# Kernel tuning notes

Measured on AMD Instinct MI355X. Metric: run time of the kernel, lower is better.

The kernel has to match this reference:

```python
import jax, jax.numpy as jnp
import numpy as np

B, S, H = 2, 2048, 1024
NH, HD = 16, 64  # num heads, head dim
EPS = 1e-12


def setup_inputs() -> dict:
    key = jax.random.key(0)
    ks = jax.random.split(key, 10)
    scale = 0.02
    return {
        "hidden_states": jax.random.normal(ks[0], (B, S, H), jnp.float32),
        "attention_mask": jnp.zeros((B, 1, 1, S), jnp.float32),
        "Wq": jax.random.normal(ks[1], (H, H), jnp.float32) * scale,
        "bq": jnp.zeros((H,), jnp.float32),
        "Wk": jax.random.normal(ks[2], (H, H), jnp.float32) * scale,
        "bk": jnp.zeros((H,), jnp.float32),
        "Wv": jax.random.normal(ks[3], (H, H), jnp.float32) * scale,
        "bv": jnp.zeros((H,), jnp.float32),
        "Wo": jax.random.normal(ks[4], (H, H), jnp.float32) * scale,
        "bo": jnp.zeros((H,), jnp.float32),
        "ln_gamma": jnp.ones((H,), jnp.float32),
        "ln_beta": jnp.zeros((H,), jnp.float32),
    }


def _split_heads(x):
    # [B,S,H] -> [B,NH,S,HD]
    b, s, _ = x.shape
    return x.reshape(b, s, NH, HD).transpose(0, 2, 1, 3)


def reference(hidden_states, attention_mask, Wq, bq, Wk, bk, Wv, bv, Wo, bo, ln_gamma, ln_beta):
    q = _split_heads(hidden_states @ Wq + bq)
    k = _split_heads(hidden_states @ Wk + bk)
    v = _split_heads(hidden_states @ Wv + bv)

    # unfused SDPA, as in source: matmul -> scale -> mask -> softmax -> matmul
    scores = jnp.einsum('bhqd,bhkd->bhqk', q, k) / jnp.sqrt(jnp.float32(HD))
    scores = scores + attention_mask
    probs = jax.nn.softmax(scores, axis=-1)  # dropout p=0 (eval)
    ctx = jnp.einsum('bhqk,bhkd->bhqd', probs, v)
    ctx = ctx.transpose(0, 2, 1, 3).reshape(hidden_states.shape)  # [B,S,H]

    # BaseBertSelfOutput: dense -> (dropout p=0) -> LayerNorm(residual)
    out = ctx @ Wo + bo
    res = out + hidden_states
    mu = jnp.mean(res, axis=-1, keepdims=True)
    var = jnp.mean(jnp.square(res - mu), axis=-1, keepdims=True)
    normed = (res - mu) * jax.lax.rsqrt(var + EPS)
    return normed * ln_gamma + ln_beta
```

## Files before the change

kernel.cpp:

```cpp
#include <hip/hip_runtime.h>
#include <hip/hip_bf16.h>

#define B_  2
#define S_  2048
#define H_  1024
#define NH_ 16
#define HD_ 64
#define EPSLN 1e-12f
#define LOG2E 1.4426950408889634f

typedef short bf16x8 __attribute__((ext_vector_type(8)));
typedef float f32x4  __attribute__((ext_vector_type(4)));

__device__ __forceinline__ float bf2f(ushort u) {
    union { unsigned int i; float f; } v; v.i = ((unsigned int)u) << 16; return v.f;
}
__device__ __forceinline__ ushort f2bf(float f) {
    union { float f; unsigned int i; } v; v.f = f;
    unsigned int r = v.i + 0x7FFFu + ((v.i >> 16) & 1u);
    return (ushort)(r >> 16);
}
__device__ __forceinline__ ushort f2bf_hw(float f) {
    __hip_bfloat16 h = __float2bfloat16(f);
    return *reinterpret_cast<ushort*>(&h);
}
__device__ __forceinline__ unsigned int pack_bf2(float a, float b) {
    return ((unsigned int)f2bf_hw(b) << 16) | (unsigned int)f2bf_hw(a);
}

__global__ __launch_bounds__(256) void cvt_f32_bf16(const float* __restrict__ in,
                                                    ushort* __restrict__ out, int n) {
    int i = (blockIdx.x * 256 + threadIdx.x) * 4;
    float4 v = *(const float4*)&in[i];
    ushort4 o = make_ushort4(f2bf(v.x), f2bf(v.y), f2bf(v.z), f2bf(v.w));
    *(ushort4*)&out[i] = o;
}

__global__ __launch_bounds__(256) void scale_mask(const float* __restrict__ in,
                                                  float* __restrict__ out) {
    int i = blockIdx.x * 256 + threadIdx.x;
    out[i] = in[i] * LOG2E;
}

__global__ __launch_bounds__(256) void transpose_cvt(
        const float* __restrict__ W0, const float* __restrict__ W1,
        const float* __restrict__ W2, const float* __restrict__ W3,
        ushort* __restrict__ T0, ushort* __restrict__ T1,
        ushort* __restrict__ T2, ushort* __restrict__ T3) {
    const int z = blockIdx.z;
    const float* in = (z == 0) ? W0 : (z == 1) ? W1 : (z == 2) ? W2 : W3;
    ushort* out     = (z == 0) ? T0 : (z == 1) ? T1 : (z == 2) ? T2 : T3;

    __shared__ float tile[64][65];
    const int bx = blockIdx.x * 64, by = blockIdx.y * 64;
    const int t = threadIdx.x;
    #pragma unroll
    for (int i = 0; i < 16; i++) {
        int idx = t + i * 256;
        int r = idx >> 6, c = idx & 63;
        tile[r][c] = in[(by + r) * 1024 + bx + c];
    }
    __syncthreads();
    #pragma unroll
    for (int i = 0; i < 16; i++) {
        int idx = t + i * 256;
        int r = idx >> 6, c = idx & 63;
        out[(bx + r) * 1024 + by + c] = f2bf(tile[c][r]);
    }
}

__global__ __launch_bounds__(256) void v_transpose(const ushort* __restrict__ Vb,
                                                   ushort* __restrict__ VtG) {
    __shared__ ushort tile[64][72];
    const int s0 = blockIdx.x * 64;
    const int head = blockIdx.y;
    const ushort* src = Vb + (size_t)head * S_ * HD_;
    ushort* dst       = VtG + (size_t)head * S_ * HD_;
    const int t = threadIdx.x, lane = t & 63, w = t >> 6;

    uint4 a = *(const uint4*)&src[(s0 + lane) * HD_ + w * 16];
    uint4 b = *(const uint4*)&src[(s0 + lane) * HD_ + w * 16 + 8];
    const ushort* pa = (const ushort*)&a;
    #pragma unroll
    for (int i = 0; i < 8; i++) tile[w * 16 + i][lane] = pa[i];
    const ushort* pb = (const ushort*)&b;
    #pragma unroll
    for (int i = 0; i < 8; i++) tile[w * 16 + 8 + i][lane] = pb[i];
    __syncthreads();

    const int d = t >> 2, sc = (t & 3) * 16;
    uint4 o1 = *(const uint4*)&tile[d][sc];
    uint4 o2 = *(const uint4*)&tile[d][sc + 8];
    *(uint4*)&dst[d * S_ + s0 + sc]     = o1;
    *(uint4*)&dst[d * S_ + s0 + sc + 8] = o2;
}

__global__ __launch_bounds__(256) void qkv_gemm(
        const ushort* __restrict__ X,
        const ushort* __restrict__ Wqt, const ushort* __restrict__ Wkt, const ushort* __restrict__ Wvt,
        const float* __restrict__ bq,  const float* __restrict__ bk,  const float* __restrict__ bv,
        ushort* __restrict__ Qo, ushort* __restrict__ Ko, ushort* __restrict__ Vo) {
    const int which = blockIdx.z;
    const ushort* Wt  = (which == 0) ? Wqt : (which == 1) ? Wkt : Wvt;
    const float* bias = (which == 0) ? bq  : (which == 1) ? bk  : bv;
    ushort* Out       = (which == 0) ? Qo  : (which == 1) ? Ko  : Vo;

    __shared__ ushort As[128][72];
    __shared__ ushort Bs[128][72];
    const int m0 = blockIdx.x * 128, n0 = blockIdx.y * 128;
    const int t = threadIdx.x;
    const int lane = t & 63, w = t >> 6;
    const int wr = (w >> 1) * 64, wc = (w & 1) * 64;
    const int l15 = lane & 15, l4 = lane >> 4;

    f32x4 acc[4][4] = {};
    const int sr = t >> 3, sc = (t & 7) * 8;

    for (int k0 = 0; k0 < H_; k0 += 64) {
        __syncthreads();
        #pragma unroll
        for (int p = 0; p < 4; p++) {
            uint4 av  = *(const uint4*)&X [(m0 + p * 32 + sr) * H_ + k0 + sc];
            uint4 bv2 = *(const uint4*)&Wt[(n0 + p * 32 + sr) * H_ + k0 + sc];
            *(uint4*)&As[p * 32 + sr][sc] = av;
            *(uint4*)&Bs[p * 32 + sr][sc] = bv2;
        }
        __syncthreads();
        #pragma unroll
        for (int ks = 0; ks < 2; ks++) {
            bf16x8 af[4], bfr[4];
            #pragma unroll
            for (int i = 0; i < 4; i++) af[i]  = *(const bf16x8*)&As[wr + i * 16 + l15][ks * 32 + l4 * 8];
            #pragma unroll
            for (int i = 0; i < 4; i++) bfr[i] = *(const bf16x8*)&Bs[wc + i * 16 + l15][ks * 32 + l4 * 8];
            #pragma unroll
            for (int mi = 0; mi < 4; mi++)
                #pragma unroll
                for (int ni = 0; ni < 4; ni++)
                    acc[mi][ni] = __builtin_amdgcn_mfma_f32_16x16x32_bf16(af[mi], bfr[ni], acc[mi][ni], 0, 0, 0);
        }
    }

    #pragma unroll
    for (int ni = 0; ni < 4; ni++) {
        int n = n0 + wc + ni * 16 + l15;
        float bvf = bias[n];
        int h = n >> 6, d = n & 63;
        #pragma unroll
        for (int mi = 0; mi < 4; mi++) {
            int mrow = m0 + wr + mi * 16 + l4 * 4;
            #pragma unroll
            for (int j = 0; j < 4; j++) {
                int m = mrow + j;
                int b = m >> 11, s = m & 2047;
                Out[((b * NH_ + h) * S_ + s) * HD_ + d] = f2bf(acc[mi][ni][j] + bvf);
            }
        }
    }
}

__global__ __launch_bounds__(256) void flash_attn(
        const ushort* __restrict__ Q, const ushort* __restrict__ K, const ushort* __restrict__ VtG,
        const float* __restrict__ maskL2, ushort* __restrict__ ctx) {
    __shared__ __align__(16) ushort Ks[64][72];
    __shared__ __align__(16) ushort Vt[64][72];
    __shared__ __align__(16) ushort Ps[4][16][72];

    const int wgid = blockIdx.x;
    const int vid  = (wgid & 7) * 128 + (wgid >> 3);
    const int qt   = vid & 31;
    const int hb   = vid >> 5;
    const int h    = hb & (NH_ - 1), b = hb >> 4;

    const int t = threadIdx.x, lane = t & 63, w = t >> 6;
    const int l15 = lane & 15, l4 = lane >> 4;
    const size_t head_off = (size_t)hb * S_ * HD_;
    const ushort* Qh = Q + head_off;
    const ushort* Kh = K + head_off;
    const ushort* Vh = VtG + head_off;

    const int qrow = qt * 64 + w * 16 + l15;
    bf16x8 qf[2];
    qf[0] = *(const bf16x8*)&Qh[qrow * 64 + 0  + l4 * 8];
    qf[1] = *(const bf16x8*)&Qh[qrow * 64 + 32 + l4 * 8];

    f32x4 ctx_acc[4] = {};
    float mrun = -1e30f, lrun = 0.f;

    const int sr  = t >> 2, sc0 = (t & 3) * 8;
    const int vsc = (t & 3) * 16;

    uint4 kr0 = *(const uint4*)&Kh[sr * 64 + sc0];
    uint4 kr1 = *(const uint4*)&Kh[sr * 64 + sc0 + 32];
    uint4 vr0 = *(const uint4*)&Vh[sr * S_ + vsc];
    uint4 vr1 = *(const uint4*)&Vh[sr * S_ + vsc + 8];

    const float ksc = 0.125f * LOG2E;

    for (int kv0 = 0; kv0 < S_; kv0 += 64) {
        __syncthreads();
        *(uint4*)&Ks[sr][sc0]      = kr0;
        *(uint4*)&Ks[sr][sc0 + 32] = kr1;
        *(uint4*)&Vt[sr][vsc]      = vr0;
        *(uint4*)&Vt[sr][vsc + 8]  = vr1;
        if (kv0 + 64 < S_) {
            kr0 = *(const uint4*)&Kh[(kv0 + 64 + sr) * 64 + sc0];
            kr1 = *(const uint4*)&Kh[(kv0 + 64 + sr) * 64 + sc0 + 32];
            vr0 = *(const uint4*)&Vh[sr * S_ + kv0 + 64 + vsc];
            vr1 = *(const uint4*)&Vh[sr * S_ + kv0 + 64 + vsc + 8];
        }
        __syncthreads();

        f32x4 sacc[4] = {};
        #pragma unroll
        for (int ks = 0; ks < 2; ks++) {
            bf16x8 kf[4];
            #pragma unroll
            for (int n = 0; n < 4; n++) kf[n] = *(const bf16x8*)&Ks[n * 16 + l15][ks * 32 + l4 * 8];
            #pragma unroll
            for (int n = 0; n < 4; n++)
                sacc[n] = __builtin_amdgcn_mfma_f32_16x16x32_bf16(kf[n], qf[ks], sacc[n], 0, 0, 0);
        }

        float tmax = -1e30f;
        #pragma unroll
        for (int n = 0; n < 4; n++) {
            float4 mk4 = *(const float4*)&maskL2[b * S_ + kv0 + n * 16 + l4 * 4];
            sacc[n][0] = fmaf(sacc[n][0], ksc, mk4.x);
            sacc[n][1] = fmaf(sacc[n][1], ksc, mk4.y);
            sacc[n][2] = fmaf(sacc[n][2], ksc, mk4.z);
            sacc[n][3] = fmaf(sacc[n][3], ksc, mk4.w);
            tmax = fmaxf(tmax, fmaxf(fmaxf(sacc[n][0], sacc[n][1]), fmaxf(sacc[n][2], sacc[n][3])));
        }
        tmax = fmaxf(tmax, __shfl_xor(tmax, 16, 64));
        tmax = fmaxf(tmax, __shfl_xor(tmax, 32, 64));

        float mnew  = fmaxf(mrun, tmax);
        float scale = exp2f(mrun - mnew);
        mrun = mnew;

        float tsum = 0.f;
        #pragma unroll
        for (int n = 0; n < 4; n++) {
            float p0 = exp2f(sacc[n][0] - mnew);
            float p1 = exp2f(sacc[n][1] - mnew);
            float p2 = exp2f(sacc[n][2] - mnew);
            float p3 = exp2f(sacc[n][3] - mnew);
            tsum += (p0 + p1) + (p2 + p3);
            uint2 pw = make_uint2(pack_bf2(p0, p1), pack_bf2(p2, p3));
            *(uint2*)&Ps[w][l15][n * 16 + l4 * 4] = pw;
        }
        tsum += __shfl_xor(tsum, 16, 64);
        tsum += __shfl_xor(tsum, 32, 64);
        lrun = lrun * scale + tsum;

        float sj[4];
        #pragma unroll
        for (int j = 0; j < 4; j++) sj[j] = __shfl(scale, l4 * 4 + j, 64);
        #pragma unroll
        for (int df = 0; df < 4; df++)
            #pragma unroll
            for (int j = 0; j < 4; j++) ctx_acc[df][j] *= sj[j];

        #pragma unroll
        for (int ks = 0; ks < 2; ks++) {
            bf16x8 pf = *(const bf16x8*)&Ps[w][l15][ks * 32 + l4 * 8];
            #pragma unroll
            for (int df = 0; df < 4; df++) {
                bf16x8 vf = *(const bf16x8*)&Vt[df * 16 + l15][ks * 32 + l4 * 8];
                ctx_acc[df] = __builtin_amdgcn_mfma_f32_16x16x32_bf16(pf, vf, ctx_acc[df], 0, 0, 0);
            }
        }
    }

    float lr[4];
    #pragma unroll
    for (int j = 0; j < 4; j++) lr[j] = 1.0f / __shfl(lrun, l4 * 4 + j, 64);
    #pragma unroll
    for (int df = 0; df < 4; df++) {
        int col = h * HD_ + df * 16 + l15;
        #pragma unroll
        for (int j = 0; j < 4; j++) {
            int s = qt * 64 + w * 16 + l4 * 4 + j;
            ctx[((size_t)b * S_ + s) * H_ + col] = f2bf(ctx_acc[df][j] * lr[j]);
        }
    }
}

__global__ __launch_bounds__(256) void out_proj(
        const ushort* __restrict__ Ctx, const ushort* __restrict__ Wot,
        const float* __restrict__ bo,  const float* __restrict__ Hs,
        float* __restrict__ Tmp) {
    __shared__ ushort As[128][72];
    __shared__ ushort Bs[128][72];
    const int m0 = blockIdx.x * 128, n0 = blockIdx.y * 128;
    const int t = threadIdx.x;
    const int lane = t & 63, w = t >> 6;
    const int wr = (w >> 1) * 64, wc = (w & 1) * 64;
    const int l15 = lane & 15, l4 = lane >> 4;

    f32x4 acc[4][4] = {};
    const int sr = t >> 3, sc = (t & 7) * 8;

    for (int k0 = 0; k0 < H_; k0 += 64) {
        __syncthreads();
        #pragma unroll
        for (int p = 0; p < 4; p++) {
            uint4 av  = *(const uint4*)&Ctx[(m0 + p * 32 + sr) * H_ + k0 + sc];
            uint4 bv2 = *(const uint4*)&Wot[(n0 + p * 32 + sr) * H_ + k0 + sc];
            *(uint4*)&As[p * 32 + sr][sc] = av;
            *(uint4*)&Bs[p * 32 + sr][sc] = bv2;
        }
        __syncthreads();
        #pragma unroll
        for (int ks = 0; ks < 2; ks++) {
            bf16x8 af[4], bfr[4];
            #pragma unroll
            for (int i = 0; i < 4; i++) af[i]  = *(const bf16x8*)&As[wr + i * 16 + l15][ks * 32 + l4 * 8];
            #pragma unroll
            for (int i = 0; i < 4; i++) bfr[i] = *(const bf16x8*)&Bs[wc + i * 16 + l15][ks * 32 + l4 * 8];
            #pragma unroll
            for (int mi = 0; mi < 4; mi++)
                #pragma unroll
                for (int ni = 0; ni < 4; ni++)
                    acc[mi][ni] = __builtin_amdgcn_mfma_f32_16x16x32_bf16(af[mi], bfr[ni], acc[mi][ni], 0, 0, 0);
        }
    }

    #pragma unroll
    for (int ni = 0; ni < 4; ni++) {
        int n = n0 + wc + ni * 16 + l15;
        float bvf = bo[n];
        #pragma unroll
        for (int mi = 0; mi < 4; mi++) {
            int mrow = m0 + wr + mi * 16 + l4 * 4;
            #pragma unroll
            for (int j = 0; j < 4; j++) {
                int m = mrow + j;
                Tmp[(size_t)m * H_ + n] = acc[mi][ni][j] + bvf + Hs[(size_t)m * H_ + n];
            }
        }
    }
}

__global__ __launch_bounds__(256) void ln_kernel(
        const float* __restrict__ Tmp, const float* __restrict__ gamma,
        const float* __restrict__ beta, float* __restrict__ Out) {
    const int row = blockIdx.x;
    const float* x = Tmp + (size_t)row * H_;
    const int t = threadIdx.x, w = t >> 6, lane = t & 63;

    float4 v = *(const float4*)&x[t * 4];
    float s = v.x + v.y + v.z + v.w;
    #pragma unroll
    for (int m = 1; m < 64; m <<= 1) s += __shfl_xor(s, m, 64);
    __shared__ float red[4], red2[4];
    if (lane == 0) red[w] = s;
    __syncthreads();
    float mu = (red[0] + red[1] + red[2] + red[3]) * (1.0f / H_);

    float d0 = v.x - mu, d1 = v.y - mu, d2 = v.z - mu, d3 = v.w - mu;
    float sq = d0 * d0 + d1 * d1 + d2 * d2 + d3 * d3;
    #pragma unroll
    for (int m = 1; m < 64; m <<= 1) sq += __shfl_xor(sq, m, 64);
    if (lane == 0) red2[w] = sq;
    __syncthreads();
    float var = (red2[0] + red2[1] + red2[2] + red2[3]) * (1.0f / H_);
    float rstd = rsqrtf(var + EPSLN);

    float dd[4] = {d0, d1, d2, d3};
    float4 o;
    o.x = dd[0] * rstd * gamma[t * 4 + 0] + beta[t * 4 + 0];
    o.y = dd[1] * rstd * gamma[t * 4 + 1] + beta[t * 4 + 1];
    o.z = dd[2] * rstd * gamma[t * 4 + 2] + beta[t * 4 + 2];
    o.w = dd[3] * rstd * gamma[t * 4 + 3] + beta[t * 4 + 3];
    *(float4*)&Out[(size_t)row * H_ + t * 4] = o;
}

extern "C" void kernel_launch(void* const* d_in, const int* in_sizes, int n_in,
                              void* d_out, int out_size, void* d_ws, size_t ws_size,
                              hipStream_t stream) {
    const float* hs    = (const float*)d_in[0];
    const float* mask  = (const float*)d_in[1];
    const float* Wq    = (const float*)d_in[2];
    const float* bq    = (const float*)d_in[3];
    const float* Wk    = (const float*)d_in[4];
    const float* bk    = (const float*)d_in[5];
    const float* Wv    = (const float*)d_in[6];
    const float* bv    = (const float*)d_in[7];
    const float* Wo    = (const float*)d_in[8];
    const float* bo    = (const float*)d_in[9];
    const float* gamma = (const float*)d_in[10];
    const float* beta  = (const float*)d_in[11];

    char* ws = (char*)d_ws;
    const size_t WSZ = (size_t)H_ * H_;
    const size_t TSZ = (size_t)B_ * S_ * H_;
    ushort* Wqt = (ushort*)ws;
    ushort* Wkt = Wqt + WSZ;
    ushort* Wvt = Wkt + WSZ;
    ushort* Wot = Wvt + WSZ;
    ushort* Xb  = Wot + WSZ;
    ushort* Qb  = Xb + TSZ;
    ushort* Kb  = Qb + TSZ;
    ushort* Vb  = Kb + TSZ;
    ushort* Ctx = Vb + TSZ;
    float*  Tmp = (float*)(Ctx + TSZ);
    ushort* VtG = (ushort*)Tmp;
    float* MaskL2 = (float*)Xb;

    cvt_f32_bf16<<<TSZ / (256 * 4), 256, 0, stream>>>(hs, Xb, (int)TSZ);
    transpose_cvt<<<dim3(16, 16, 4), 256, 0, stream>>>(Wq, Wk, Wv, Wo, Wqt, Wkt, Wvt, Wot);

    qkv_gemm<<<dim3(32, 8, 3), 256, 0, stream>>>(Xb, Wqt, Wkt, Wvt, bq, bk, bv, Qb, Kb, Vb);
    scale_mask<<<(B_ * S_) / 256, 256, 0, stream>>>(mask, MaskL2);
    v_transpose<<<dim3(S_ / 64, B_ * NH_), 256, 0, stream>>>(Vb, VtG);
    flash_attn<<<dim3(1024), 256, 0, stream>>>(Qb, Kb, VtG, MaskL2, Ctx);
    out_proj<<<dim3(32, 8), 256, 0, stream>>>(Ctx, Wot, bo, hs, Tmp);
    ln_kernel<<<B_ * S_, 256, 0, stream>>>(Tmp, gamma, beta, (float*)d_out);
}
```

Before: 176.0 us.

## Rewrite flash attention with 32x32 MFMA, register-resident P, and lazy rescaling

Flash attention now uses 32x32x16 MFMA tiles with 2 waves of 32 query rows each (128 threads) instead of 4 waves using 16x16 tiles. The probability tile is passed from the QK^T accumulator to the PV MFMA operand through cross-lane shuffles rather than a round trip through shared memory. The running max is only rescaled when a tile's max exceeds it by more than 8 (log2 units), which skips most accumulator rescales. The intent is to cut LDS traffic, shuffles and VALU work per KV tile. In exchange there is more register pressure, half as many threads per block, and larger unnormalised exponentials (bounded by 2^8).

After: 287.3 us. +63.2%, slower.

```diff
diff --git a/kernel.cpp b/kernel.cpp
--- a/kernel.cpp
+++ b/kernel.cpp
@@ -11,6 +11,8 @@
 
 typedef short bf16x8 __attribute__((ext_vector_type(8)));
 typedef float f32x4  __attribute__((ext_vector_type(4)));
+typedef float f32x16 __attribute__((ext_vector_type(16)));
+typedef unsigned int u32x4 __attribute__((ext_vector_type(4)));
 
 __device__ __forceinline__ float bf2f(ushort u) {
     union { unsigned int i; float f; } v; v.i = ((unsigned int)u) << 16; return v.f;
@@ -159,12 +161,11 @@
     }
 }
 
-__global__ __launch_bounds__(256) void flash_attn(
+__global__ __launch_bounds__(128) void flash_attn(
         const ushort* __restrict__ Q, const ushort* __restrict__ K, const ushort* __restrict__ VtG,
         const float* __restrict__ maskL2, ushort* __restrict__ ctx) {
     __shared__ __align__(16) ushort Ks[64][72];
     __shared__ __align__(16) ushort Vt[64][72];
-    __shared__ __align__(16) ushort Ps[4][16][72];
 
     const int wgid = blockIdx.x;
     const int vid  = (wgid & 7) * 128 + (wgid >> 3);
@@ -173,117 +174,138 @@
     const int h    = hb & (NH_ - 1), b = hb >> 4;
 
     const int t = threadIdx.x, lane = t & 63, w = t >> 6;
-    const int l15 = lane & 15, l4 = lane >> 4;
+    const int l31 = lane & 31, hi = lane >> 5;
     const size_t head_off = (size_t)hb * S_ * HD_;
     const ushort* Qh = Q + head_off;
     const ushort* Kh = K + head_off;
     const ushort* Vh = VtG + head_off;
 
-    const int qrow = qt * 64 + w * 16 + l15;
-    bf16x8 qf[2];
-    qf[0] = *(const bf16x8*)&Qh[qrow * 64 + 0  + l4 * 8];
-    qf[1] = *(const bf16x8*)&Qh[qrow * 64 + 32 + l4 * 8];
-
-    f32x4 ctx_acc[4] = {};
+    const int q0w  = qt * 64 + w * 32;
+    const int qrow = q0w + l31;
+    bf16x8 qf[4];
+    #pragma unroll
+    for (int kc = 0; kc < 4; kc++)
+        qf[kc] = *(const bf16x8*)&Qh[qrow * 64 + kc * 16 + hi * 8];
+
+    f32x16 acc0 = {}, acc1 = {};
     float mrun = -1e30f, lrun = 0.f;
 
-    const int sr  = t >> 2, sc0 = (t & 3) * 8;
-    const int vsc = (t & 3) * 16;
-
-    uint4 kr0 = *(const uint4*)&Kh[sr * 64 + sc0];
-    uint4 kr1 = *(const uint4*)&Kh[sr * 64 + sc0 + 32];
-    uint4 vr0 = *(const uint4*)&Vh[sr * S_ + vsc];
-    uint4 vr1 = *(const uint4*)&Vh[sr * S_ + vsc + 8];
+    uint4 kpre[4], vpre[4];
+    #pragma unroll
+    for (int it = 0; it < 4; it++) {
+        int ci = it * 128 + t;
+        int row = ci >> 3, ce = (ci & 7) * 8;
+        kpre[it] = *(const uint4*)&Kh[row * 64 + ce];
+        vpre[it] = *(const uint4*)&Vh[row * S_ + ce];
+    }
 
     const float ksc = 0.125f * LOG2E;
 
     for (int kv0 = 0; kv0 < S_; kv0 += 64) {
         __syncthreads();
-        *(uint4*)&Ks[sr][sc0]      = kr0;
-        *(uint4*)&Ks[sr][sc0 + 32] = kr1;
-        *(uint4*)&Vt[sr][vsc]      = vr0;
-        *(uint4*)&Vt[sr][vsc + 8]  = vr1;
+        #pragma unroll
+        for (int it = 0; it < 4; it++) {
+            int ci = it * 128 + t;
+            int row = ci >> 3, ce = (ci & 7) * 8;
+            *(uint4*)&Ks[row][ce] = kpre[it];
+            *(uint4*)&Vt[row][ce] = vpre[it];
+        }
         if (kv0 + 64 < S_) {
-            kr0 = *(const uint4*)&Kh[(kv0 + 64 + sr) * 64 + sc0];
-            kr1 = *(const uint4*)&Kh[(kv0 + 64 + sr) * 64 + sc0 + 32];
-            vr0 = *(const uint4*)&Vh[sr * S_ + kv0 + 64 + vsc];
-            vr1 = *(const uint4*)&Vh[sr * S_ + kv0 + 64 + vsc + 8];
-        }
-        __syncthreads();
-
-        f32x4 sacc[4] = {};
-        #pragma unroll
-        for (int ks = 0; ks < 2; ks++) {
-            bf16x8 kf[4];
-            #pragma unroll
-            for (int n = 0; n < 4; n++) kf[n] = *(const bf16x8*)&Ks[n * 16 + l15][ks * 32 + l4 * 8];
-            #pragma unroll
-            for (int n = 0; n < 4; n++)
-                sacc[n] = __builtin_amdgcn_mfma_f32_16x16x32_bf16(kf[n], qf[ks], sacc[n], 0, 0, 0);
+            #pragma unroll
+            for (int it = 0; it < 4; it++) {
+                int ci = it * 128 + t;
+                int row = ci >> 3, ce = (ci & 7) * 8;
+                kpre[it] = *(const uint4*)&Kh[(kv0 + 64 + row) * 64 + ce];
+                vpre[it] = *(const uint4*)&Vh[row * S_ + kv0 + 64 + ce];
+            }
+        }
+        __syncthreads();
+
+        f32x16 s0 = {}, s1 = {};
+        #pragma unroll
+        for (int kc = 0; kc < 4; kc++) {
+            bf16x8 kf0 = *(const bf16x8*)&Ks[l31][kc * 16 + hi * 8];
+            bf16x8 kf1 = *(const bf16x8*)&Ks[32 + l31][kc * 16 + hi * 8];
+            s0 = __builtin_amdgcn_mfma_f32_32x32x16_bf16(kf0, qf[kc], s0, 0, 0, 0);
+            s1 = __builtin_amdgcn_mfma_f32_32x32x16_bf16(kf1, qf[kc], s1, 0, 0, 0);
         }
 
         float tmax = -1e30f;
         #pragma unroll
-        for (int n = 0; n < 4; n++) {
-            float4 mk4 = *(const float4*)&maskL2[b * S_ + kv0 + n * 16 + l4 * 4];
-            sacc[n][0] = fmaf(sacc[n][0], ksc, mk4.x);
-            sacc[n][1] = fmaf(sacc[n][1], ksc, mk4.y);
-            sacc[n][2] = fmaf(sacc[n][2], ksc, mk4.z);
-            sacc[n][3] = fmaf(sacc[n][3], ksc, mk4.w);
-            tmax = fmaxf(tmax, fmaxf(fmaxf(sacc[n][0], sacc[n][1]), fmaxf(sacc[n][2], sacc[n][3])));
-        }
-        tmax = fmaxf(tmax, __shfl_xor(tmax, 16, 64));
+        for (int g = 0; g < 4; g++) {
+            float4 mk0 = *(const float4*)&maskL2[b * S_ + kv0 + g * 8 + hi * 4];
+            float4 mk1 = *(const float4*)&maskL2[b * S_ + kv0 + 32 + g * 8 + hi * 4];
+            #pragma unroll
+            for (int j = 0; j < 4; j++) {
+                int r = g * 4 + j;
+                s0[r] = fmaf(s0[r], ksc, (&mk0.x)[j]);
+                s1[r] = fmaf(s1[r], ksc, (&mk1.x)[j]);
+                tmax = fmaxf(tmax, fmaxf(s0[r], s1[r]));
+            }
+        }
         tmax = fmaxf(tmax, __shfl_xor(tmax, 32, 64));
 
-        float mnew  = fmaxf(mrun, tmax);
-        float scale = exp2f(mrun - mnew);
-        mrun = mnew;
-
+        if (!__all(tmax <= mrun + 8.0f)) {
+            float mnew  = fmaxf(mrun, tmax);
+            float scale = exp2f(mrun - mnew);
+            mrun = mnew;
+            lrun *= scale;
+            #pragma unroll
+            for (int r = 0; r < 16; r++) { acc0[r] *= scale; acc1[r] *= scale; }
+        }
+
+        float e0[16], e1[16];
         float tsum = 0.f;
         #pragma unroll
-        for (int n = 0; n < 4; n++) {
-            float p0 = exp2f(sacc[n][0] - mnew);
-            float p1 = exp2f(sacc[n][1] - mnew);
-            float p2 = exp2f(sacc[n][2] - mnew);
-            float p3 = exp2f(sacc[n][3] - mnew);
-            tsum += (p0 + p1) + (p2 + p3);
-            uint2 pw = make_uint2(pack_bf2(p0, p1), pack_bf2(p2, p3));
-            *(uint2*)&Ps[w][l15][n * 16 + l4 * 4] = pw;
-        }
-        tsum += __shfl_xor(tsum, 16, 64);
+        for (int r = 0; r < 16; r++) {
+            e0[r] = exp2f(s0[r] - mrun);
+            e1[r] = exp2f(s1[r] - mrun);
+            tsum += e0[r] + e1[r];
+        }
         tsum += __shfl_xor(tsum, 32, 64);
-        lrun = lrun * scale + tsum;
-
-        float sj[4];
-        #pragma unroll
-        for (int j = 0; j < 4; j++) sj[j] = __shfl(scale, l4 * 4 + j, 64);
-        #pragma unroll
-        for (int df = 0; df < 4; df++)
-            #pragma unroll
-            for (int j = 0; j < 4; j++) ctx_acc[df][j] *= sj[j];
-
-        #pragma unroll
-        for (int ks = 0; ks < 2; ks++) {
-            bf16x8 pf = *(const bf16x8*)&Ps[w][l15][ks * 32 + l4 * 8];
-            #pragma unroll
-            for (int df = 0; df < 4; df++) {
-                bf16x8 vf = *(const bf16x8*)&Vt[df * 16 + l15][ks * 32 + l4 * 8];
-                ctx_acc[df] = __builtin_amdgcn_mfma_f32_16x16x32_bf16(pf, vf, ctx_acc[df], 0, 0, 0);
-            }
-        }
-    }
-
-    float lr[4];
-    #pragma unroll
-    for (int j = 0; j < 4; j++) lr[j] = 1.0f / __shfl(lrun, l4 * 4 + j, 64);
-    #pragma unroll
-    for (int df = 0; df < 4; df++) {
-        int col = h * HD_ + df * 16 + l15;
-        #pragma unroll
-        for (int j = 0; j < 4; j++) {
-            int s = qt * 64 + w * 16 + l4 * 4 + j;
-            ctx[((size_t)b * S_ + s) * H_ + col] = f2bf(ctx_acc[df][j] * lr[j]);
-        }
+        lrun += tsum;
+
+        bf16x8 pf[4];
+        #pragma unroll
+        for (int c = 0; c < 4; c++) {
+            const float* e = (c >> 1) ? e1 : e0;
+            int u = c & 1;
+            unsigned int Lo0 = pack_bf2(e[8 * u + 0], e[8 * u + 1]);
+            unsigned int Lo1 = pack_bf2(e[8 * u + 2], e[8 * u + 3]);
+            unsigned int Hi0 = pack_bf2(e[8 * u + 4], e[8 * u + 5]);
+            unsigned int Hi1 = pack_bf2(e[8 * u + 6], e[8 * u + 7]);
+            unsigned int sLo0 = (unsigned int)__shfl_xor((int)Lo0, 32, 64);
+            unsigned int sLo1 = (unsigned int)__shfl_xor((int)Lo1, 32, 64);
+            unsigned int sHi0 = (unsigned int)__shfl_xor((int)Hi0, 32, 64);
+            unsigned int sHi1 = (unsigned int)__shfl_xor((int)Hi1, 32, 64);
+            u32x4 d;
+            d.x = hi ? sHi0 : Lo0;
+            d.y = hi ? sHi1 : Lo1;
+            d.z = hi ? Hi0 : sLo0;
+            d.w = hi ? Hi1 : sLo1;
+            pf[c] = __builtin_bit_cast(bf16x8, d);
+        }
+
+        #pragma unroll
+        for (int c = 0; c < 4; c++) {
+            bf16x8 vf0 = *(const bf16x8*)&Vt[l31][c * 16 + hi * 8];
+            bf16x8 vf1 = *(const bf16x8*)&Vt[32 + l31][c * 16 + hi * 8];
+            acc0 = __builtin_amdgcn_mfma_f32_32x32x16_bf16(vf0, pf[c], acc0, 0, 0, 0);
+            acc1 = __builtin_amdgcn_mfma_f32_32x32x16_bf16(vf1, pf[c], acc1, 0, 0, 0);
+        }
+    }
+
+    const float inv = 1.0f / lrun;
+    const size_t rowbase = ((size_t)b * S_ + q0w + l31) * H_ + h * 64;
+    #pragma unroll
+    for (int g = 0; g < 4; g++) {
+        ushort4 o0, o1;
+        o0.x = f2bf(acc0[g * 4 + 0] * inv); o0.y = f2bf(acc0[g * 4 + 1] * inv);
+        o0.z = f2bf(acc0[g * 4 + 2] * inv); o0.w = f2bf(acc0[g * 4 + 3] * inv);
+        o1.x = f2bf(acc1[g * 4 + 0] * inv); o1.y = f2bf(acc1[g * 4 + 1] * inv);
+        o1.z = f2bf(acc1[g * 4 + 2] * inv); o1.w = f2bf(acc1[g * 4 + 3] * inv);
+        *(ushort4*)&ctx[rowbase + g * 8 + hi * 4]      = o0;
+        *(ushort4*)&ctx[rowbase + 32 + g * 8 + hi * 4] = o1;
     }
 }
 
@@ -415,7 +437,7 @@
     qkv_gemm<<<dim3(32, 8, 3), 256, 0, stream>>>(Xb, Wqt, Wkt, Wvt, bq, bk, bv, Qb, Kb, Vb);
     scale_mask<<<(B_ * S_) / 256, 256, 0, stream>>>(mask, MaskL2);
     v_transpose<<<dim3(S_ / 64, B_ * NH_), 256, 0, stream>>>(Vb, VtG);
-    flash_attn<<<dim3(1024), 256, 0, stream>>>(Qb, Kb, VtG, MaskL2, Ctx);
+    flash_attn<<<dim3(1024), 128, 0, stream>>>(Qb, Kb, VtG, MaskL2, Ctx);
     out_proj<<<dim3(32, 8), 256, 0, stream>>>(Ctx, Wot, bo, hs, Tmp);
     ln_kernel<<<B_ * S_, 256, 0, stream>>>(Tmp, gamma, beta, (float*)d_out);
 }
```
